# Kernel tuning notes

Hardware: AMD Instinct MI355X
Metric: run time of the kernel (lower is better)

## Reference

```python
import jax, jax.numpy as jnp
import numpy as np

BS, NQ, NC = 64, 3000, 256
FH, FW, TOPK = 100, 100, 1500
INK_INF = jnp.float32(1e20)


def setup_inputs() -> dict:
    key = jax.random.key(0)
    k1, k2, k3 = jax.random.split(key, 3)
    u = jax.random.uniform(k1, (BS, NQ, 4), dtype=jnp.float32)
    # cx,cy in [0.25,0.75], w,h in [0,0.4] -> xyxy strictly inside [0,1]
    cxcy = 0.25 + 0.5 * u[..., :2]
    wh = 0.4 * u[..., 2:]
    output_coord = jnp.concatenate([cxcy, wh], axis=-1)
    output_class = jax.random.uniform(k2, (BS, NQ, NC), dtype=jnp.float32)
    # valid feature extent [valid_h, valid_w] per image (from ~mask cumsum in original)
    valid_feature_size = jax.random.randint(k3, (BS, 2), 50, FH + 1, dtype=jnp.int32)
    rows = jnp.arange(FH)[None, :, None]
    cols = jnp.arange(FW)[None, None, :]
    padding_mask = (rows >= valid_feature_size[:, 0][:, None, None]) | (
        cols >= valid_feature_size[:, 1][:, None, None]
    )  # (BS, FH, FW) bool, True = padded
    return {
        "output_coord": output_coord,
        "output_class": output_class,
        "valid_feature_size": valid_feature_size,
        "padding_mask": padding_mask,
        "feature_h": FH,
        "feature_w": FW,
        "topk": TOPK,
    }


def reference(output_coord, output_class, valid_feature_size, padding_mask,
              feature_h, feature_w, topk):
    bs = output_coord.shape[0]
    # scores = output_class.max(dim=-1); topk box select
    scores = jnp.max(output_class, axis=-1)                      # (bs, nq)
    _, topk_idx = jax.lax.top_k(scores, topk)                    # (bs, k)
    boxes = jnp.take_along_axis(output_coord, topk_idx[..., None], axis=1)  # (bs,k,4) cxcywh
    # box_cxcywh_to_xyxy
    cxcy, wh = boxes[..., :2], boxes[..., 2:]
    xyxy = jnp.concatenate([cxcy - 0.5 * wh, cxcy + 0.5 * wh], axis=-1)  # (bs,k,4)
    # valid_size.repeat(1,2) -> [vh, vw, vh, vw]
    vfs = valid_feature_size.astype(xyxy.dtype)
    scale = jnp.concatenate([vfs, vfs], axis=-1)[:, None, :]     # (bs,1,4)
    rng = jnp.floor(xyxy * scale).astype(jnp.int32)              # (bs,k,4)
    lx, ly, rx, ry = rng[..., 0], rng[..., 1], rng[..., 2], rng[..., 3]
    rows = jnp.arange(feature_h)
    cols = jnp.arange(feature_w)
    # per-box row/col membership; union over boxes via batched GEMM
    R = ((rows[None, None, :] >= ly[..., None]) & (rows[None, None, :] < ry[..., None])).astype(jnp.float32)  # (bs,k,h)
    C = ((cols[None, None, :] >= lx[..., None]) & (cols[None, None, :] < rx[..., None])).astype(jnp.float32)  # (bs,k,w)
    covered = jnp.einsum('bkh,bkw->bhw', R, C) > 0               # (bs,h,w)
    extra_mask = ~covered                                        # True outside every kept box
    # mask = extra_mask | padding_mask; float masked_fill(-INK_INF)
    full = extra_mask.reshape(bs, -1) | padding_mask.reshape(bs, -1)
    attn_mask = jnp.where(full, -INK_INF, jnp.float32(0.0))      # (bs, h*w)
    return attn_mask
```

## Files before the change

### kernel.cpp

```cpp
#include <hip/hip_runtime.h>

#define BS   64
#define NQ   3000
#define NC   256
#define FH   100
#define FW   100
#define TOPK 1500

__global__ __launch_bounds__(256) void scores_kernel(const float4* __restrict__ cls,
                                                     float* __restrict__ scores) {
    const int tid  = threadIdx.x;
    const int lane = tid & 63;
    const int wave = tid >> 6;
    const int row0 = blockIdx.x * 16 + wave * 4;
    const float4* p = cls + (size_t)row0 * (NC / 4) + lane;
    float4 a = p[0], b = p[64], c = p[128], d = p[192];
    float m0 = fmaxf(fmaxf(a.x, a.y), fmaxf(a.z, a.w));
    float m1 = fmaxf(fmaxf(b.x, b.y), fmaxf(b.z, b.w));
    float m2 = fmaxf(fmaxf(c.x, c.y), fmaxf(c.z, c.w));
    float m3 = fmaxf(fmaxf(d.x, d.y), fmaxf(d.z, d.w));
#pragma unroll
    for (int off = 32; off > 0; off >>= 1) {
        m0 = fmaxf(m0, __shfl_xor(m0, off, 64));
        m1 = fmaxf(m1, __shfl_xor(m1, off, 64));
        m2 = fmaxf(m2, __shfl_xor(m2, off, 64));
        m3 = fmaxf(m3, __shfl_xor(m3, off, 64));
    }
    if (lane < 4) {
        float m = (lane == 0) ? m0 : (lane == 1) ? m1 : (lane == 2) ? m2 : m3;
        scores[row0 + lane] = m;
    }
}

#define NTM 512

__global__ __launch_bounds__(NTM) void mask_kernel(const float4* __restrict__ coord,
                                                   const int* __restrict__ vfs,
                                                   const float* __restrict__ scores,
                                                   float* __restrict__ out) {
    __shared__ unsigned su[NQ];
    __shared__ int      hist[8][256];
    __shared__ unsigned cov[FH * 4];
    __shared__ int      eqlist[NQ];
    __shared__ int      wave_sum[4];
    __shared__ int      s_selbin, s_K, s_ecnt;

    const int b    = blockIdx.x;
    const int tid  = threadIdx.x;
    const int wid  = tid >> 6;

    for (int q = tid; q < NQ; q += NTM)
        su[q] = __float_as_uint(scores[b * NQ + q]);
    for (int i = tid; i < FH * 4; i += NTM) cov[i] = 0u;
    if (tid == 0) s_ecnt = 0;

    unsigned prefix = 0, pmask = 0;
    int K = TOPK;
#pragma unroll
    for (int p = 0; p < 4; ++p) {
        const int shift = 24 - 8 * p;
        for (int i = tid; i < 8 * 256; i += NTM) ((int*)hist)[i] = 0;
        __syncthreads();
        for (int q = tid; q < NQ; q += NTM) {
            unsigned u = su[q];
            if ((u & pmask) == prefix)
                atomicAdd(&hist[wid][(u >> shift) & 0xFF], 1);
        }
        __syncthreads();
        int x = 0, hx = 0, bin = 0;
        if (tid < 256) {
            bin = 255 - tid;
            hx = hist[0][bin] + hist[1][bin] + hist[2][bin] + hist[3][bin] +
                 hist[4][bin] + hist[5][bin] + hist[6][bin] + hist[7][bin];
            x = hx;
#pragma unroll
            for (int off = 1; off < 64; off <<= 1) {
                int y = __shfl_up(x, off, 64);
                if ((tid & 63) >= off) x += y;
            }
            if ((tid & 63) == 63) wave_sum[tid >> 6] = x;
        }
        __syncthreads();
        if (tid < 256) {
            int w = tid >> 6;
            for (int j = 0; j < w; ++j) x += wave_sum[j];
            int ge_incl = x;
            int ge_excl = x - hx;
            if (ge_incl >= K && ge_excl < K) {
                s_selbin = bin;
                s_K      = K - ge_excl;
            }
        }
        __syncthreads();
        prefix |= ((unsigned)s_selbin) << shift;
        pmask  |= (0xFFu << shift);
        K = s_K;
        __syncthreads();
    }
    const unsigned v      = prefix;
    const int      e_take = K;

    const float s0 = (float)vfs[2 * b];
    const float s1 = (float)vfs[2 * b + 1];

    for (int q = tid; q < NQ; q += NTM) {
        unsigned u = su[q];
        if (u > v) {
            float4 c4 = coord[(size_t)b * NQ + q];
            float x1 = c4.x - 0.5f * c4.z, y1 = c4.y - 0.5f * c4.w;
            float x2 = c4.x + 0.5f * c4.z, y2 = c4.y + 0.5f * c4.w;
            int lx = (int)floorf(x1 * s0), ly = (int)floorf(y1 * s1);
            int rx = (int)floorf(x2 * s0), ry = (int)floorf(y2 * s1);
            int h0 = ly > 0 ? ly : 0, h1 = ry < FH ? ry : FH;
            int w0 = lx > 0 ? lx : 0, w1 = rx < FW ? rx : FW;
            if (h0 < h1 && w0 < w1) {
                unsigned m[4];
#pragma unroll
                for (int j = 0; j < 4; ++j) {
                    int lo = w0 - 32 * j; lo = lo < 0 ? 0 : lo;
                    int hi = w1 - 32 * j; hi = hi > 32 ? 32 : hi;
                    unsigned mm = 0u;
                    if (hi > lo) {
                        unsigned top = (hi >= 32) ? 0xFFFFFFFFu : ((1u << hi) - 1u);
                        unsigned bot = (lo <= 0) ? 0u : ((1u << lo) - 1u);
                        mm = top & ~bot;
                    }
                    m[j] = mm;
                }
                for (int h = h0; h < h1; ++h) {
#pragma unroll
                    for (int j = 0; j < 4; ++j)
                        if (m[j]) atomicOr(&cov[h * 4 + j], m[j]);
                }
            }
        } else if (u == v) {
            int i = atomicAdd(&s_ecnt, 1);
            eqlist[i] = q;
        }
    }
    __syncthreads();

    const int E = s_ecnt;
    for (int i = tid; i < E; i += NTM) {
        int q = eqlist[i];
        int r = 0;
        for (int j = 0; j < E; ++j) r += (eqlist[j] < q) ? 1 : 0;
        if (r < e_take) {
            float4 c4 = coord[(size_t)b * NQ + q];
            float x1 = c4.x - 0.5f * c4.z, y1 = c4.y - 0.5f * c4.w;
            float x2 = c4.x + 0.5f * c4.z, y2 = c4.y + 0.5f * c4.w;
            int lx = (int)floorf(x1 * s0), ly = (int)floorf(y1 * s1);
            int rx = (int)floorf(x2 * s0), ry = (int)floorf(y2 * s1);
            int h0 = ly > 0 ? ly : 0, h1 = ry < FH ? ry : FH;
            int w0 = lx > 0 ? lx : 0, w1 = rx < FW ? rx : FW;
            if (h0 < h1 && w0 < w1) {
                for (int h = h0; h < h1; ++h) {
#pragma unroll
                    for (int j = 0; j < 4; ++j) {
                        int lo = w0 - 32 * j; lo = lo < 0 ? 0 : lo;
                        int hi = w1 - 32 * j; hi = hi > 32 ? 32 : hi;
                        if (hi > lo) {
                            unsigned top = (hi >= 32) ? 0xFFFFFFFFu : ((1u << hi) - 1u);
                            unsigned bot = (lo <= 0) ? 0u : ((1u << lo) - 1u);
                            atomicOr(&cov[h * 4 + j], top & ~bot);
                        }
                    }
                }
            }
        }
    }
    __syncthreads();

    const int iv0 = vfs[2 * b], iv1 = vfs[2 * b + 1];
    for (int idx = tid; idx < FH * FW; idx += NTM) {
        int h = idx / FW;
        int w = idx - h * FW;
        bool covered = (cov[h * 4 + (w >> 5)] >> (w & 31)) & 1u;
        bool pad = (h >= iv0) || (w >= iv1);
        out[(size_t)b * (FH * FW) + idx] = (covered && !pad) ? 0.0f : -1e20f;
    }
}

extern "C" void kernel_launch(void* const* d_in, const int* in_sizes, int n_in,
                              void* d_out, int out_size, void* d_ws, size_t ws_size,
                              hipStream_t stream) {
    const float4* coord = (const float4*)d_in[0];
    const float*  cls   = (const float*)d_in[1];
    const int*    vfs   = (const int*)d_in[2];
    float* scores = (float*)d_ws;
    float* out    = (float*)d_out;

    const int rows = BS * NQ;
    scores_kernel<<<rows / 16, 256, 0, stream>>>((const float4*)cls, scores);
    mask_kernel<<<BS, NTM, 0, stream>>>(coord, vfs, scores, out);
}
```

Baseline: 319.6 us.

## Split per-image box rasterization across blocks and merge coverage in an emit kernel

The single per-image mask kernel becomes a raster kernel launched over (NSPLIT, BS) blocks. Each block repeats the radix top-k threshold selection, then rasterizes only its slice of queries into a partial coverage bitmap in workspace. Tie handling changes: the equal-score list is ranked once to find a query-index cutoff, so ties are handled in the main loop instead of a second rasterization pass. A separate elementwise emit kernel ORs the partial bitmaps and writes the output. This raises parallelism beyond 64 blocks, at the cost of recomputing the selection in every block, an extra kernel launch and extra workspace traffic.

```diff
diff --git a/kernel.cpp b/kernel.cpp
--- a/kernel.cpp
+++ b/kernel.cpp
@@ -32,20 +32,23 @@
     }
 }
 
-#define NTM 512
+#define NSPLIT 8
+#define NTM    512
+#define QSLICE ((NQ + NSPLIT - 1) / NSPLIT)
 
-__global__ __launch_bounds__(NTM) void mask_kernel(const float4* __restrict__ coord,
-                                                   const int* __restrict__ vfs,
-                                                   const float* __restrict__ scores,
-                                                   float* __restrict__ out) {
+__global__ __launch_bounds__(NTM) void raster_kernel(const float4* __restrict__ coord,
+                                                     const int* __restrict__ vfs,
+                                                     const float* __restrict__ scores,
+                                                     unsigned* __restrict__ pcov) {
     __shared__ unsigned su[NQ];
     __shared__ int      hist[8][256];
     __shared__ unsigned cov[FH * 4];
     __shared__ int      eqlist[NQ];
     __shared__ int      wave_sum[4];
-    __shared__ int      s_selbin, s_K, s_ecnt;
+    __shared__ int      s_selbin, s_K, s_ecnt, s_qcut;
 
-    const int b    = blockIdx.x;
+    const int part = blockIdx.x;
+    const int b    = blockIdx.y;
     const int tid  = threadIdx.x;
     const int wid  = tid >> 6;
 
@@ -100,12 +103,27 @@
     const unsigned v      = prefix;
     const int      e_take = K;
 
+    for (int q = tid; q < NQ; q += NTM)
+        if (su[q] == v) { int i = atomicAdd(&s_ecnt, 1); eqlist[i] = q; }
+    __syncthreads();
+    const int E = s_ecnt;
+    for (int i = tid; i < E; i += NTM) {
+        int q = eqlist[i];
+        int r = 0;
+        for (int j = 0; j < E; ++j) r += (eqlist[j] < q) ? 1 : 0;
+        if (r == e_take - 1) s_qcut = q + 1;
+    }
+    __syncthreads();
+    const int qcut = s_qcut;
+
     const float s0 = (float)vfs[2 * b];
     const float s1 = (float)vfs[2 * b + 1];
 
-    for (int q = tid; q < NQ; q += NTM) {
+    const int q0 = part * QSLICE;
+    const int q1 = (q0 + QSLICE < NQ) ? (q0 + QSLICE) : NQ;
+    for (int q = q0 + tid; q < q1; q += NTM) {
         unsigned u = su[q];
-        if (u > v) {
+        if (u > v || (u == v && q < qcut)) {
             float4 c4 = coord[(size_t)b * NQ + q];
             float x1 = c4.x - 0.5f * c4.z, y1 = c4.y - 0.5f * c4.w;
             float x2 = c4.x + 0.5f * c4.z, y2 = c4.y + 0.5f * c4.w;
@@ -133,52 +151,30 @@
                         if (m[j]) atomicOr(&cov[h * 4 + j], m[j]);
                 }
             }
-        } else if (u == v) {
-            int i = atomicAdd(&s_ecnt, 1);
-            eqlist[i] = q;
         }
     }
     __syncthreads();
 
-    const int E = s_ecnt;
-    for (int i = tid; i < E; i += NTM) {
-        int q = eqlist[i];
-        int r = 0;
-        for (int j = 0; j < E; ++j) r += (eqlist[j] < q) ? 1 : 0;
-        if (r < e_take) {
-            float4 c4 = coord[(size_t)b * NQ + q];
-            float x1 = c4.x - 0.5f * c4.z, y1 = c4.y - 0.5f * c4.w;
-            float x2 = c4.x + 0.5f * c4.z, y2 = c4.y + 0.5f * c4.w;
-            int lx = (int)floorf(x1 * s0), ly = (int)floorf(y1 * s1);
-            int rx = (int)floorf(x2 * s0), ry = (int)floorf(y2 * s1);
-            int h0 = ly > 0 ? ly : 0, h1 = ry < FH ? ry : FH;
-            int w0 = lx > 0 ? lx : 0, w1 = rx < FW ? rx : FW;
-            if (h0 < h1 && w0 < w1) {
-                for (int h = h0; h < h1; ++h) {
+    unsigned* dst = pcov + (size_t)(b * NSPLIT + part) * (FH * 4);
+    for (int i = tid; i < FH * 4; i += NTM) dst[i] = cov[i];
+}
+
+__global__ __launch_bounds__(256) void emit_kernel(const unsigned* __restrict__ pcov,
+                                                   const int* __restrict__ vfs,
+                                                   float* __restrict__ out) {
+    const int idx = blockIdx.x * 256 + threadIdx.x;
+    if (idx >= BS * FH * FW) return;
+    const int b    = idx / (FH * FW);
+    const int cell = idx - b * (FH * FW);
+    const int h    = cell / FW;
+    const int w    = cell - h * FW;
+    const unsigned* p = pcov + (size_t)b * NSPLIT * (FH * 4) + h * 4 + (w >> 5);
+    unsigned acc = 0u;
 #pragma unroll
-                    for (int j = 0; j < 4; ++j) {
-                        int lo = w0 - 32 * j; lo = lo < 0 ? 0 : lo;
-                        int hi = w1 - 32 * j; hi = hi > 32 ? 32 : hi;
-                        if (hi > lo) {
-                            unsigned top = (hi >= 32) ? 0xFFFFFFFFu : ((1u << hi) - 1u);
-                            unsigned bot = (lo <= 0) ? 0u : ((1u << lo) - 1u);
-                            atomicOr(&cov[h * 4 + j], top & ~bot);
-                        }
-                    }
-                }
-            }
-        }
-    }
-    __syncthreads();
-
-    const int iv0 = vfs[2 * b], iv1 = vfs[2 * b + 1];
-    for (int idx = tid; idx < FH * FW; idx += NTM) {
-        int h = idx / FW;
-        int w = idx - h * FW;
-        bool covered = (cov[h * 4 + (w >> 5)] >> (w & 31)) & 1u;
-        bool pad = (h >= iv0) || (w >= iv1);
-        out[(size_t)b * (FH * FW) + idx] = (covered && !pad) ? 0.0f : -1e20f;
-    }
+    for (int s = 0; s < NSPLIT; ++s) acc |= p[s * (FH * 4)];
+    const bool covered = (acc >> (w & 31)) & 1u;
+    const bool pad     = (h >= vfs[2 * b]) || (w >= vfs[2 * b + 1]);
+    out[idx] = (covered && !pad) ? 0.0f : -1e20f;
 }
 
 extern "C" void kernel_launch(void* const* d_in, const int* in_sizes, int n_in,
@@ -187,10 +183,12 @@
     const float4* coord = (const float4*)d_in[0];
     const float*  cls   = (const float*)d_in[1];
     const int*    vfs   = (const int*)d_in[2];
-    float* scores = (float*)d_ws;
-    float* out    = (float*)d_out;
+    float*    scores = (float*)d_ws;
+    unsigned* pcov   = (unsigned*)((char*)d_ws + (size_t)BS * NQ * sizeof(float));
+    float* out = (float*)d_out;
 
     const int rows = BS * NQ;
     scores_kernel<<<rows / 16, 256, 0, stream>>>((const float4*)cls, scores);
-    mask_kernel<<<BS, NTM, 0, stream>>>(coord, vfs, scores, out);
+    raster_kernel<<<dim3(NSPLIT, BS), NTM, 0, stream>>>(coord, vfs, scores, pcov);
+    emit_kernel<<<(BS * FH * FW) / 256, 256, 0, stream>>>(pcov, vfs, out);
 }
```

Result: faster. 301.3 us (-5.7%).

## Split mask kernel into row stripes per batch and resolve top-k ties by cutoff

Applied to the files above, without the earlier changes.

The mask kernel now runs as an 8x64 grid, each block rasterizing only a 13-row stripe of the coverage map. That raises parallelism from 64 blocks to 512 on a GPU with many CUs. Every stripe block repeats the radix top-k select, and tie handling now computes a query-index cutoff instead of running a separate atomic pass. Score loads and output stores are vectorized to 16-byte accesses. The trade-off is eightfold redundant selection work per image.

```diff
diff --git a/kernel.cpp b/kernel.cpp
--- a/kernel.cpp
+++ b/kernel.cpp
@@ -32,27 +32,35 @@
     }
 }
 
-#define NTM 512
+#define NSTRIPE 8
+#define RPS     13
+#define NTM     512
 
-__global__ __launch_bounds__(NTM) void mask_kernel(const float4* __restrict__ coord,
-                                                   const int* __restrict__ vfs,
-                                                   const float* __restrict__ scores,
-                                                   float* __restrict__ out) {
-    __shared__ unsigned su[NQ];
+__global__ __launch_bounds__(NTM) void raster_kernel(const float4* __restrict__ coord,
+                                                     const int* __restrict__ vfs,
+                                                     const float* __restrict__ scores,
+                                                     float* __restrict__ out) {
+    __shared__ __align__(16) unsigned su[NQ];
     __shared__ int      hist[8][256];
-    __shared__ unsigned cov[FH * 4];
     __shared__ int      eqlist[NQ];
+    __shared__ unsigned cov[RPS * 4];
     __shared__ int      wave_sum[4];
-    __shared__ int      s_selbin, s_K, s_ecnt;
+    __shared__ int      s_selbin, s_K, s_c24, s_qcut;
 
-    const int b    = blockIdx.x;
+    const int part = blockIdx.x;
+    const int b    = blockIdx.y;
     const int tid  = threadIdx.x;
     const int wid  = tid >> 6;
+    const int r0   = part * RPS;
+    const int r1   = (r0 + RPS < FH) ? (r0 + RPS) : FH;
 
-    for (int q = tid; q < NQ; q += NTM)
-        su[q] = __float_as_uint(scores[b * NQ + q]);
-    for (int i = tid; i < FH * 4; i += NTM) cov[i] = 0u;
-    if (tid == 0) s_ecnt = 0;
+    {
+        const uint4* sp = (const uint4*)(scores + b * NQ);
+        uint4* sd = (uint4*)su;
+        for (int i = tid; i < NQ / 4; i += NTM) sd[i] = sp[i];
+    }
+    if (tid < RPS * 4) cov[tid] = 0u;
+    if (tid == 0) s_c24 = 0;
 
     unsigned prefix = 0, pmask = 0;
     int K = TOPK;
@@ -63,8 +71,10 @@
         __syncthreads();
         for (int q = tid; q < NQ; q += NTM) {
             unsigned u = su[q];
-            if ((u & pmask) == prefix)
+            if ((u & pmask) == prefix) {
+                if (p == 3) eqlist[atomicAdd(&s_c24, 1)] = q;
                 atomicAdd(&hist[wid][(u >> shift) & 0xFF], 1);
+            }
         }
         __syncthreads();
         int x = 0, hx = 0, bin = 0;
@@ -100,19 +110,34 @@
     const unsigned v      = prefix;
     const int      e_take = K;
 
+    const int C24 = s_c24;
+    for (int i = tid; i < C24; i += NTM) {
+        int q = eqlist[i];
+        if (su[q] == v) {
+            int r = 0;
+            for (int j = 0; j < C24; ++j) {
+                int qj = eqlist[j];
+                r += (su[qj] == v && qj < q) ? 1 : 0;
+            }
+            if (r == e_take - 1) s_qcut = q + 1;
+        }
+    }
+    __syncthreads();
+    const int qcut = s_qcut;
+
     const float s0 = (float)vfs[2 * b];
     const float s1 = (float)vfs[2 * b + 1];
 
     for (int q = tid; q < NQ; q += NTM) {
         unsigned u = su[q];
-        if (u > v) {
+        if (u > v || (u == v && q < qcut)) {
             float4 c4 = coord[(size_t)b * NQ + q];
             float x1 = c4.x - 0.5f * c4.z, y1 = c4.y - 0.5f * c4.w;
             float x2 = c4.x + 0.5f * c4.z, y2 = c4.y + 0.5f * c4.w;
             int lx = (int)floorf(x1 * s0), ly = (int)floorf(y1 * s1);
             int rx = (int)floorf(x2 * s0), ry = (int)floorf(y2 * s1);
-            int h0 = ly > 0 ? ly : 0, h1 = ry < FH ? ry : FH;
-            int w0 = lx > 0 ? lx : 0, w1 = rx < FW ? rx : FW;
+            int h0 = ly > r0 ? ly : r0, h1 = ry < r1 ? ry : r1;
+            int w0 = lx > 0 ? lx : 0,   w1 = rx < FW ? rx : FW;
             if (h0 < h1 && w0 < w1) {
                 unsigned m[4];
 #pragma unroll
@@ -130,41 +155,7 @@
                 for (int h = h0; h < h1; ++h) {
 #pragma unroll
                     for (int j = 0; j < 4; ++j)
-                        if (m[j]) atomicOr(&cov[h * 4 + j], m[j]);
-                }
-            }
-        } else if (u == v) {
-            int i = atomicAdd(&s_ecnt, 1);
-            eqlist[i] = q;
-        }
-    }
-    __syncthreads();
-
-    const int E = s_ecnt;
-    for (int i = tid; i < E; i += NTM) {
-        int q = eqlist[i];
-        int r = 0;
-        for (int j = 0; j < E; ++j) r += (eqlist[j] < q) ? 1 : 0;
-        if (r < e_take) {
-            float4 c4 = coord[(size_t)b * NQ + q];
-            float x1 = c4.x - 0.5f * c4.z, y1 = c4.y - 0.5f * c4.w;
-            float x2 = c4.x + 0.5f * c4.z, y2 = c4.y + 0.5f * c4.w;
-            int lx = (int)floorf(x1 * s0), ly = (int)floorf(y1 * s1);
-            int rx = (int)floorf(x2 * s0), ry = (int)floorf(y2 * s1);
-            int h0 = ly > 0 ? ly : 0, h1 = ry < FH ? ry : FH;
-            int w0 = lx > 0 ? lx : 0, w1 = rx < FW ? rx : FW;
-            if (h0 < h1 && w0 < w1) {
-                for (int h = h0; h < h1; ++h) {
-#pragma unroll
-                    for (int j = 0; j < 4; ++j) {
-                        int lo = w0 - 32 * j; lo = lo < 0 ? 0 : lo;
-                        int hi = w1 - 32 * j; hi = hi > 32 ? 32 : hi;
-                        if (hi > lo) {
-                            unsigned top = (hi >= 32) ? 0xFFFFFFFFu : ((1u << hi) - 1u);
-                            unsigned bot = (lo <= 0) ? 0u : ((1u << lo) - 1u);
-                            atomicOr(&cov[h * 4 + j], top & ~bot);
-                        }
-                    }
+                        if (m[j]) atomicOr(&cov[(h - r0) * 4 + j], m[j]);
                 }
             }
         }
@@ -172,12 +163,21 @@
     __syncthreads();
 
     const int iv0 = vfs[2 * b], iv1 = vfs[2 * b + 1];
-    for (int idx = tid; idx < FH * FW; idx += NTM) {
-        int h = idx / FW;
-        int w = idx - h * FW;
-        bool covered = (cov[h * 4 + (w >> 5)] >> (w & 31)) & 1u;
-        bool pad = (h >= iv0) || (w >= iv1);
-        out[(size_t)b * (FH * FW) + idx] = (covered && !pad) ? 0.0f : -1e20f;
+    const int nrow = r1 - r0;
+    float4* out4 = (float4*)(out + (size_t)b * (FH * FW));
+    for (int idx = tid; idx < nrow * (FW / 4); idx += NTM) {
+        const int hr = idx / (FW / 4);
+        const int w4 = idx - hr * (FW / 4);
+        const int h  = r0 + hr;
+        const int w  = w4 * 4;
+        const unsigned word = cov[hr * 4 + (w >> 5)];
+        const bool padr = (h >= iv0);
+        float4 o;
+        o.x = (((word >> ((w + 0) & 31)) & 1u) && !(padr || (w + 0 >= iv1))) ? 0.0f : -1e20f;
+        o.y = (((word >> ((w + 1) & 31)) & 1u) && !(padr || (w + 1 >= iv1))) ? 0.0f : -1e20f;
+        o.z = (((word >> ((w + 2) & 31)) & 1u) && !(padr || (w + 2 >= iv1))) ? 0.0f : -1e20f;
+        o.w = (((word >> ((w + 3) & 31)) & 1u) && !(padr || (w + 3 >= iv1))) ? 0.0f : -1e20f;
+        out4[h * (FW / 4) + w4] = o;
     }
 }
 
@@ -192,5 +192,5 @@
 
     const int rows = BS * NQ;
     scores_kernel<<<rows / 16, 256, 0, stream>>>((const float4*)cls, scores);
-    mask_kernel<<<BS, NTM, 0, stream>>>(coord, vfs, scores, out);
+    raster_kernel<<<dim3(NSTRIPE, BS), NTM, 0, stream>>>(coord, vfs, scores, out);
 }
```

After: 309.0 us. 3.3% less time.
